# Kernel optimization log

Hardware: AMD Instinct MI355X
Metric: run time of the kernel (lower is better)

## Reference

```python
import jax, jax.numpy as jnp
import numpy as np

N_NODES = 50000
N_EDGES = 800000
EPS = 0.1

def setup_inputs() -> dict:
    key = jax.random.key(0)
    ks = jax.random.split(key, 6)
    x = jax.random.normal(ks[0], (N_NODES, 256), dtype=jnp.float32)
    edge_index = jax.random.randint(ks[1], (2, N_EDGES), 0, N_NODES, dtype=jnp.int64)
    W1 = jax.random.normal(ks[2], (256, 64), dtype=jnp.float32) * (1.0 / np.sqrt(256))
    b1 = jnp.zeros((64,), dtype=jnp.float32)
    att = jax.random.normal(ks[3], (2, 1, 64), dtype=jnp.float32) * (1.0 / np.sqrt(64))
    W2 = jax.random.normal(ks[4], (64, 16), dtype=jnp.float32) * (1.0 / np.sqrt(64))
    b2 = jnp.zeros((16,), dtype=jnp.float32)
    return {"x": x, "edge_index": edge_index, "W1": W1, "b1": b1, "att": att, "W2": W2, "b2": b2}

def _fagcn_conv(x, row, col, norm, att_l, eps):
    # message: norm * x_j gathered at source (row), scatter-add to target (col)
    msg = norm[:, None] * x[row]                      # [E_tot, H]
    x_l = jax.ops.segment_sum(msg, col, num_segments=N_NODES)  # low-pass
    x_h = -eps * x_l                                   # high-pass message = -eps * low message
    gate = jax.nn.sigmoid(jnp.sum(x * att_l, axis=-1, keepdims=True))  # [N,1]
    return gate * x_l + (1.0 - gate) * x_h

def reference(x, edge_index, W1, b1, att, W2, b2):
    # add self loops once (same edge set is reused by every layer)
    loops = jnp.arange(N_NODES, dtype=edge_index.dtype)
    row = jnp.concatenate([edge_index[0], loops])
    col = jnp.concatenate([edge_index[1], loops])
    deg = jax.ops.segment_sum(jnp.ones_like(col, dtype=x.dtype), col, num_segments=N_NODES)
    dinv = jnp.where(deg > 0, jax.lax.rsqrt(jnp.maximum(deg, 1e-30)), 0.0)
    norm = dinv[row] * dinv[col]                       # [E_tot]
    # eval mode: dropout is identity
    h = jax.nn.relu(x @ W1 + b1)                       # [N, H]
    for l in range(att.shape[0]):
        h = _fagcn_conv(h, row, col, norm, att[l], EPS)
    return h @ W2 + b2                                 # [N, out]
```

## Files before the change

### kernel.cpp

```cpp
#include <hip/hip_runtime.h>
#include <math.h>

#define N_FEAT_IN 256
#define N_HID 64
#define N_OUT 16
#define EPS 0.1f

typedef short bf16x8 __attribute__((ext_vector_type(8)));
typedef float f32x4 __attribute__((ext_vector_type(4)));

__device__ inline uint pack2(ushort a, ushort b) { return (uint)a | ((uint)b << 16); }

__device__ inline ushort bf16_rne(float x) {
    uint b = __float_as_uint(x);
    b += 0x7fff + ((b >> 16) & 1);
    return (ushort)(b >> 16);
}

__device__ inline float blo(uint u) { return __uint_as_float(u << 16); }
__device__ inline float bhi(uint u) { return __uint_as_float(u & 0xffff0000u); }

__device__ inline void split_bf16(float x, ushort& hi, ushort& lo) {
    uint b = __float_as_uint(x);
    hi = (ushort)(b >> 16);
    float xl = x - __uint_as_float(b & 0xffff0000u);
    lo = (ushort)(__float_as_uint(xl) >> 16);
}


__global__ void zero_int(int* __restrict__ p, int n) {
    int i = blockIdx.x * blockDim.x + threadIdx.x;
    if (i < n) p[i] = 0;
}


__global__ void hist_rank(const int* __restrict__ col, const int* __restrict__ row,
                          int* __restrict__ cnt, uint* __restrict__ rr, int E) {
    int e = blockIdx.x * blockDim.x + threadIdx.x;
    if (e < E) {
        int r = atomicAdd(&cnt[col[e]], 1);
        rr[e] = ((uint)r << 16) | (uint)row[e];
    }
}


__global__ void scan_chunks(const int* __restrict__ cnt, int* __restrict__ rowptr,
                            int* __restrict__ partial, float* __restrict__ dinv, int N) {
    __shared__ int sm[256];
    int tid = threadIdx.x;
    int gid = blockIdx.x * 256 + tid;
    int v = (gid < N) ? cnt[gid] : 0;
    sm[tid] = v;
    __syncthreads();
#pragma unroll
    for (int off = 1; off < 256; off <<= 1) {
        int add = (tid >= off) ? sm[tid - off] : 0;
        __syncthreads();
        sm[tid] += add;
        __syncthreads();
    }
    if (gid < N) {
        rowptr[gid] = sm[tid] - v;
        dinv[gid] = rsqrtf(1.0f + (float)v);
    }
    if (tid == 255) partial[blockIdx.x] = sm[255];
}


__global__ void scan_finish(int* __restrict__ rowptr, const int* __restrict__ partial,
                            int N, int E, int nchunks) {
    __shared__ int sm[256];
    int tid = threadIdx.x;
    sm[tid] = (tid < nchunks) ? partial[tid] : 0;
    __syncthreads();
#pragma unroll
    for (int off = 1; off < 256; off <<= 1) {
        int add = (tid >= off) ? sm[tid - off] : 0;
        __syncthreads();
        sm[tid] += add;
        __syncthreads();
    }
    int boff = (blockIdx.x == 0) ? 0 : sm[blockIdx.x - 1];
    __syncthreads();
    int gid = blockIdx.x * 256 + tid;
    if (gid < N) rowptr[gid] += boff;
    if (gid == 0) rowptr[N] = E;
}


__global__ void csr_scatter_part(const int* __restrict__ col, const uint* __restrict__ rr,
                                 const int* __restrict__ rowptr,
                                 ushort* __restrict__ srcidx, int E, int rangeSz) {
    int r = blockIdx.x & 7;
    int nsl = gridDim.x >> 3;
    int s = blockIdx.x >> 3;
    int lo = r * rangeSz;
    int hi = lo + rangeSz;
    int stride = nsl * blockDim.x;
    for (int e = s * blockDim.x + threadIdx.x; e < E; e += stride) {
        int c = col[e];
        if (c >= lo && c < hi) {
            uint v = rr[e];
            srcidx[rowptr[c] + (v >> 16)] = (ushort)(v & 0xffffu);
        }
    }
}


__global__ __launch_bounds__(256) void gemm1_mfma(const float* __restrict__ x,
                                                  const float* __restrict__ W1,
                                                  const float* __restrict__ b1,
                                                  const float* __restrict__ dinv,
                                                  uint* __restrict__ AsOut,
                                                  int MB, int totalWaves) {
    __shared__ uint4 wh_lds[2048];
    __shared__ uint4 wl_lds[2048];
    int tid = threadIdx.x;
    for (int e = tid; e < 2048; e += 256) {
        int ks = e >> 8;
        int rem = e & 255;
        int nt = rem >> 6;
        int ln = rem & 63;
        int k0 = ks * 32 + ((ln >> 4) << 3);
        int colw = nt * 16 + (ln & 15);
        ushort hi[8], lo[8];
#pragma unroll
        for (int i = 0; i < 8; ++i) {
            float v = W1[(k0 + i) * 64 + colw];
            split_bf16(v, hi[i], lo[i]);
        }
        wh_lds[e] = make_uint4(pack2(hi[0], hi[1]), pack2(hi[2], hi[3]),
                               pack2(hi[4], hi[5]), pack2(hi[6], hi[7]));
        wl_lds[e] = make_uint4(pack2(lo[0], lo[1]), pack2(lo[2], lo[3]),
                               pack2(lo[4], lo[5]), pack2(lo[6], lo[7]));
    }
    __syncthreads();

    int lane = tid & 63;
    int m = lane & 15;
    int kg = lane >> 4;
    int wid = blockIdx.x * 4 + (tid >> 6);
    const bf16x8* whf = reinterpret_cast<const bf16x8*>(wh_lds);
    const bf16x8* wlf = reinterpret_cast<const bf16x8*>(wl_lds);
    float bias[4];
#pragma unroll
    for (int nt = 0; nt < 4; ++nt) bias[nt] = b1[nt * 16 + m];

    auto load_tile = [&](float4* dst, int mbv) {
        const float4* xr = reinterpret_cast<const float4*>(x) +
                           (size_t)(mbv * 16 + m) * 64 + kg * 2;
#pragma unroll
        for (int ks = 0; ks < 8; ++ks) {
            dst[2 * ks]     = xr[ks * 8];
            dst[2 * ks + 1] = xr[ks * 8 + 1];
        }
    };

    int mb = wid;
    if (mb >= MB) return;
    float4 xv[16], xn[16];
    load_tile(xv, mb);

    while (true) {
        int mbn = mb + totalWaves;
        bool has_next = (mbn < MB);
        if (has_next) load_tile(xn, mbn);

        f32x4 acc[4] = {{0.f,0.f,0.f,0.f},{0.f,0.f,0.f,0.f},
                        {0.f,0.f,0.f,0.f},{0.f,0.f,0.f,0.f}};
#pragma unroll
        for (int ks = 0; ks < 8; ++ks) {
            float4 a0 = xv[2 * ks];
            float4 a1 = xv[2 * ks + 1];
            float f[8] = {a0.x, a0.y, a0.z, a0.w, a1.x, a1.y, a1.z, a1.w};
            bf16x8 ah, al;
#pragma unroll
            for (int i = 0; i < 8; ++i) {
                ushort hu, lu;
                split_bf16(f[i], hu, lu);
                ah[i] = (short)hu;
                al[i] = (short)lu;
            }
#pragma unroll
            for (int nt = 0; nt < 4; ++nt) {
                bf16x8 wh = whf[(ks * 4 + nt) * 64 + lane];
                bf16x8 wl = wlf[(ks * 4 + nt) * 64 + lane];
                acc[nt] = __builtin_amdgcn_mfma_f32_16x16x32_bf16(ah, wh, acc[nt], 0, 0, 0);
                acc[nt] = __builtin_amdgcn_mfma_f32_16x16x32_bf16(al, wh, acc[nt], 0, 0, 0);
                acc[nt] = __builtin_amdgcn_mfma_f32_16x16x32_bf16(ah, wl, acc[nt], 0, 0, 0);
            }
        }

        int r0 = mb * 16 + kg * 4;
        float dr[4];
#pragma unroll
        for (int j = 0; j < 4; ++j) dr[j] = dinv[r0 + j];
#pragma unroll
        for (int nt = 0; nt < 4; ++nt) {
#pragma unroll
            for (int j = 0; j < 4; ++j) {
                float v = fmaxf(acc[nt][j] + bias[nt], 0.0f) * dr[j];
                float p = __shfl_xor(v, 1, 64);
                if ((m & 1) == 0) {
                    uint u = pack2(bf16_rne(v), bf16_rne(p));
                    AsOut[(size_t)(r0 + j) * 32 + ((nt * 16 + m) >> 1)] = u;
                }
            }
        }

        if (!has_next) break;
#pragma unroll
        for (int u = 0; u < 16; ++u) xv[u] = xn[u];
        mb = mbn;
    }
}


template <bool LAST>
__global__ __launch_bounds__(256) void fagcn_layer(
    const uint4* __restrict__ As4, uint4* __restrict__ Out4,
    const float* __restrict__ dinv, const int* __restrict__ rowptr,
    const ushort* __restrict__ src, const float* __restrict__ att_l,
    const float* __restrict__ W2, const float* __restrict__ b2,
    float* __restrict__ out, int N) {
    __shared__ float W2s[64 * 16];
    __shared__ float hL[32 * 68];
    int tid = threadIdx.x;
    if (LAST) {
        for (int e = tid; e < 64 * 16; e += 256) W2s[e] = W2[e];
        __syncthreads();
    }
    int sub = tid & 7;
    int lnode = tid >> 3;
    int i = blockIdx.x * 32 + lnode;
    if (i >= N) i = N - 1;

    int start = rowptr[i];
    int end = rowptr[i + 1];
    const uint4* Ab = As4 + sub;
    uint4 su = Ab[(size_t)i * 8];
    float s0 = blo(su.x), s1 = bhi(su.x), s2 = blo(su.y), s3 = bhi(su.y);
    float s4 = blo(su.z), s5 = bhi(su.z), s6 = blo(su.w), s7 = bhi(su.w);

    float aA0=0.f,aA1=0.f,aA2=0.f,aA3=0.f,aA4=0.f,aA5=0.f,aA6=0.f,aA7=0.f;
    float aB0=0.f,aB1=0.f,aB2=0.f,aB3=0.f,aB4=0.f,aB5=0.f,aB6=0.f,aB7=0.f;
    int j = start;
    for (; j + 7 < end; j += 8) {
        int e0 = src[j];
        int e1 = src[j + 1];
        int e2 = src[j + 2];
        int e3 = src[j + 3];
        int e4 = src[j + 4];
        int e5 = src[j + 5];
        int e6 = src[j + 6];
        int e7 = src[j + 7];
        uint4 u0 = Ab[(size_t)e0 * 8];
        uint4 u1 = Ab[(size_t)e1 * 8];
        uint4 u2 = Ab[(size_t)e2 * 8];
        uint4 u3 = Ab[(size_t)e3 * 8];
        uint4 u4 = Ab[(size_t)e4 * 8];
        uint4 u5 = Ab[(size_t)e5 * 8];
        uint4 u6 = Ab[(size_t)e6 * 8];
        uint4 u7 = Ab[(size_t)e7 * 8];
        aA0 += blo(u0.x); aA1 += bhi(u0.x); aA2 += blo(u0.y); aA3 += bhi(u0.y);
        aA4 += blo(u0.z); aA5 += bhi(u0.z); aA6 += blo(u0.w); aA7 += bhi(u0.w);
        aB0 += blo(u1.x); aB1 += bhi(u1.x); aB2 += blo(u1.y); aB3 += bhi(u1.y);
        aB4 += blo(u1.z); aB5 += bhi(u1.z); aB6 += blo(u1.w); aB7 += bhi(u1.w);
        aA0 += blo(u2.x); aA1 += bhi(u2.x); aA2 += blo(u2.y); aA3 += bhi(u2.y);
        aA4 += blo(u2.z); aA5 += bhi(u2.z); aA6 += blo(u2.w); aA7 += bhi(u2.w);
        aB0 += blo(u3.x); aB1 += bhi(u3.x); aB2 += blo(u3.y); aB3 += bhi(u3.y);
        aB4 += blo(u3.z); aB5 += bhi(u3.z); aB6 += blo(u3.w); aB7 += bhi(u3.w);
        aA0 += blo(u4.x); aA1 += bhi(u4.x); aA2 += blo(u4.y); aA3 += bhi(u4.y);
        aA4 += blo(u4.z); aA5 += bhi(u4.z); aA6 += blo(u4.w); aA7 += bhi(u4.w);
        aB0 += blo(u5.x); aB1 += bhi(u5.x); aB2 += blo(u5.y); aB3 += bhi(u5.y);
        aB4 += blo(u5.z); aB5 += bhi(u5.z); aB6 += blo(u5.w); aB7 += bhi(u5.w);
        aA0 += blo(u6.x); aA1 += bhi(u6.x); aA2 += blo(u6.y); aA3 += bhi(u6.y);
        aA4 += blo(u6.z); aA5 += bhi(u6.z); aA6 += blo(u6.w); aA7 += bhi(u6.w);
        aB0 += blo(u7.x); aB1 += bhi(u7.x); aB2 += blo(u7.y); aB3 += bhi(u7.y);
        aB4 += blo(u7.z); aB5 += bhi(u7.z); aB6 += blo(u7.w); aB7 += bhi(u7.w);
    }
    for (; j + 3 < end; j += 4) {
        int e0 = src[j];
        int e1 = src[j + 1];
        int e2 = src[j + 2];
        int e3 = src[j + 3];
        uint4 u0 = Ab[(size_t)e0 * 8];
        uint4 u1 = Ab[(size_t)e1 * 8];
        uint4 u2 = Ab[(size_t)e2 * 8];
        uint4 u3 = Ab[(size_t)e3 * 8];
        aA0 += blo(u0.x); aA1 += bhi(u0.x); aA2 += blo(u0.y); aA3 += bhi(u0.y);
        aA4 += blo(u0.z); aA5 += bhi(u0.z); aA6 += blo(u0.w); aA7 += bhi(u0.w);
        aB0 += blo(u1.x); aB1 += bhi(u1.x); aB2 += blo(u1.y); aB3 += bhi(u1.y);
        aB4 += blo(u1.z); aB5 += bhi(u1.z); aB6 += blo(u1.w); aB7 += bhi(u1.w);
        aA0 += blo(u2.x); aA1 += bhi(u2.x); aA2 += blo(u2.y); aA3 += bhi(u2.y);
        aA4 += blo(u2.z); aA5 += bhi(u2.z); aA6 += blo(u2.w); aA7 += bhi(u2.w);
        aB0 += blo(u3.x); aB1 += bhi(u3.x); aB2 += blo(u3.y); aB3 += bhi(u3.y);
        aB4 += blo(u3.z); aB5 += bhi(u3.z); aB6 += blo(u3.w); aB7 += bhi(u3.w);
    }
    for (; j < end; ++j) {
        int s = src[j];
        uint4 u = Ab[(size_t)s * 8];
        aA0 += blo(u.x); aA1 += bhi(u.x); aA2 += blo(u.y); aA3 += bhi(u.y);
        aA4 += blo(u.z); aA5 += bhi(u.z); aA6 += blo(u.w); aA7 += bhi(u.w);
    }
    float c0 = aA0 + aB0, c1 = aA1 + aB1, c2 = aA2 + aB2, c3 = aA3 + aB3;
    float c4 = aA4 + aB4, c5 = aA5 + aB5, c6 = aA6 + aB6, c7 = aA7 + aB7;

    float d = dinv[i];
    float4 at0 = reinterpret_cast<const float4*>(att_l)[2 * sub];
    float4 at1 = reinterpret_cast<const float4*>(att_l)[2 * sub + 1];
    float prod = s0 * at0.x + s1 * at0.y + s2 * at0.z + s3 * at0.w +
                 s4 * at1.x + s5 * at1.y + s6 * at1.z + s7 * at1.w;
#pragma unroll
    for (int off = 4; off > 0; off >>= 1)
        prod += __shfl_xor(prod, off, 64);
    float gate = 1.0f / (1.0f + expf(-prod / d));
    float factor = gate * (1.0f + EPS) - EPS;
    float df = d * factor;
    float h0 = df * (c0 + s0), h1 = df * (c1 + s1);
    float h2 = df * (c2 + s2), h3 = df * (c3 + s3);
    float h4 = df * (c4 + s4), h5 = df * (c5 + s5);
    float h6 = df * (c6 + s6), h7 = df * (c7 + s7);

    if (!LAST) {
        Out4[(size_t)i * 8 + sub] =
            make_uint4(pack2(bf16_rne(d * h0), bf16_rne(d * h1)),
                       pack2(bf16_rne(d * h2), bf16_rne(d * h3)),
                       pack2(bf16_rne(d * h4), bf16_rne(d * h5)),
                       pack2(bf16_rne(d * h6), bf16_rne(d * h7)));
    } else {
        float4* hrow4 = reinterpret_cast<float4*>(&hL[lnode * 68]);
        hrow4[2 * sub]     = make_float4(h0, h1, h2, h3);
        hrow4[2 * sub + 1] = make_float4(h4, h5, h6, h7);
        __syncthreads();
        const float4* h4p = reinterpret_cast<const float4*>(&hL[lnode * 68]);
        float accA = b2[sub];
        float accB = b2[sub + 8];
#pragma unroll
        for (int k4 = 0; k4 < 16; ++k4) {
            float4 hv = h4p[k4];
            int k = 4 * k4;
            accA = fmaf(hv.x, W2s[(k + 0) * 16 + sub], accA);
            accB = fmaf(hv.x, W2s[(k + 0) * 16 + sub + 8], accB);
            accA = fmaf(hv.y, W2s[(k + 1) * 16 + sub], accA);
            accB = fmaf(hv.y, W2s[(k + 1) * 16 + sub + 8], accB);
            accA = fmaf(hv.z, W2s[(k + 2) * 16 + sub], accA);
            accB = fmaf(hv.z, W2s[(k + 2) * 16 + sub + 8], accB);
            accA = fmaf(hv.w, W2s[(k + 3) * 16 + sub], accA);
            accB = fmaf(hv.w, W2s[(k + 3) * 16 + sub + 8], accB);
        }
        out[(size_t)i * 16 + sub] = accA;
        out[(size_t)i * 16 + sub + 8] = accB;
    }
}

extern "C" void kernel_launch(void* const* d_in, const int* in_sizes, int n_in,
                              void* d_out, int out_size, void* d_ws, size_t ws_size,
                              hipStream_t stream) {
    const float* x   = (const float*)d_in[0];
    const int*   ei  = (const int*)d_in[1];
    const float* W1  = (const float*)d_in[2];
    const float* b1  = (const float*)d_in[3];
    const float* att = (const float*)d_in[4];
    const float* W2  = (const float*)d_in[5];
    const float* b2  = (const float*)d_in[6];
    float* out = (float*)d_out;

    const int N = in_sizes[0] / N_FEAT_IN;
    const int E = in_sizes[1] / 2;
    const int L = in_sizes[4] / N_HID;

    const int* row = ei;
    const int* col = ei + E;

    char* wp = (char*)d_ws;
    auto alloc = [&](size_t bytes) -> char* {
        char* p = wp;
        wp += (bytes + 255) & ~(size_t)255;
        return p;
    };
    float*  dinv    = (float*)alloc((size_t)N * 4);
    int*    cnt     = (int*)alloc((size_t)N * 4);
    int*    rowptr  = (int*)alloc((size_t)(N + 1) * 4);
    uint*   rr      = (uint*)alloc((size_t)E * 4);
    int*    partial = (int*)alloc(256 * 4);
    ushort* srcidx  = (ushort*)alloc((size_t)E * 2);
    uint*   AsA     = (uint*)alloc((size_t)N * 32 * 4);
    uint*   AsB     = (uint*)alloc((size_t)N * 32 * 4);

    const int TB = 256;
    const int nchunks = (N + TB - 1) / TB;
    const int rangeSz = (N + 7) / 8;
    const int PART_GRID = 1024;

    zero_int<<<(N + TB - 1) / TB, TB, 0, stream>>>(cnt, N);
    hist_rank<<<(E + TB - 1) / TB, TB, 0, stream>>>(col, row, cnt, rr, E);
    scan_chunks<<<nchunks, TB, 0, stream>>>(cnt, rowptr, partial, dinv, N);
    scan_finish<<<nchunks, TB, 0, stream>>>(rowptr, partial, N, E, nchunks);
    csr_scatter_part<<<PART_GRID, TB, 0, stream>>>(col, rr, rowptr, srcidx, E, rangeSz);

    {
        const int blocks = 512;
        const int MB = N / 16;
        gemm1_mfma<<<blocks, TB, 0, stream>>>(x, W1, b1, dinv, AsA, MB, blocks * 4);
    }

    {
        int grid = (N + 31) / 32;
        uint4* A = (uint4*)AsA;
        uint4* B = (uint4*)AsB;
        for (int l = 0; l < L; ++l) {
            const float* att_l = att + (size_t)l * N_HID;
            if (l == L - 1) {
                fagcn_layer<true><<<grid, TB, 0, stream>>>(
                    A, B, dinv, rowptr, srcidx, att_l, W2, b2, out, N);
            } else {
                fagcn_layer<false><<<grid, TB, 0, stream>>>(
                    A, B, dinv, rowptr, srcidx, att_l, W2, b2, out, N);
                uint4* tmp = A; A = B; B = tmp;
            }
        }
    }
}
```

Baseline: 132.8 us.

## Sort nodes by in-degree so each wave aggregates similar-degree neighbourhoods

```diff
diff --git a/kernel.cpp b/kernel.cpp
--- a/kernel.cpp
+++ b/kernel.cpp
@@ -5,6 +5,7 @@
 #define N_HID 64
 #define N_OUT 16
 #define EPS 0.1f
+#define NBINS 1024
 
 typedef short bf16x8 __attribute__((ext_vector_type(8)));
 typedef float f32x4 __attribute__((ext_vector_type(4)));
@@ -45,11 +46,16 @@
 
 
 __global__ void scan_chunks(const int* __restrict__ cnt, int* __restrict__ rowptr,
-                            int* __restrict__ partial, float* __restrict__ dinv, int N) {
+                            int* __restrict__ partial, float* __restrict__ dinv,
+                            int* __restrict__ dhist, int N) {
     __shared__ int sm[256];
+    __shared__ int h[NBINS];
     int tid = threadIdx.x;
+    for (int b = tid; b < NBINS; b += 256) h[b] = 0;
+    __syncthreads();
     int gid = blockIdx.x * 256 + tid;
     int v = (gid < N) ? cnt[gid] : 0;
+    if (gid < N) atomicAdd(&h[min(v, NBINS - 1)], 1);
     sm[tid] = v;
     __syncthreads();
 #pragma unroll
@@ -64,6 +70,9 @@
         dinv[gid] = rsqrtf(1.0f + (float)v);
     }
     if (tid == 255) partial[blockIdx.x] = sm[255];
+    __syncthreads();
+    for (int b = tid; b < NBINS; b += 256)
+        if (h[b]) atomicAdd(&dhist[b], h[b]);
 }
 
 
@@ -85,6 +94,53 @@
     int gid = blockIdx.x * 256 + tid;
     if (gid < N) rowptr[gid] += boff;
     if (gid == 0) rowptr[N] = E;
+}
+
+
+__global__ void deg_scan(int* __restrict__ dhist) {
+    __shared__ int sums[256];
+    int t = threadIdx.x;
+    int v0 = dhist[4 * t], v1 = dhist[4 * t + 1];
+    int v2 = dhist[4 * t + 2], v3 = dhist[4 * t + 3];
+    int s = v0 + v1 + v2 + v3;
+    sums[t] = s;
+    __syncthreads();
+#pragma unroll
+    for (int off = 1; off < 256; off <<= 1) {
+        int add = (t >= off) ? sums[t - off] : 0;
+        __syncthreads();
+        sums[t] += add;
+        __syncthreads();
+    }
+    int excl = sums[t] - s;
+    dhist[4 * t]     = excl;
+    dhist[4 * t + 1] = excl + v0;
+    dhist[4 * t + 2] = excl + v0 + v1;
+    dhist[4 * t + 3] = excl + v0 + v1 + v2;
+}
+
+
+__global__ void perm_scatter(const int* __restrict__ cnt, int* __restrict__ dbase,
+                             int* __restrict__ perm, int N) {
+    __shared__ int h[NBINS];
+    __shared__ int hb[NBINS];
+    int tid = threadIdx.x;
+    for (int b = tid; b < NBINS; b += 256) h[b] = 0;
+    __syncthreads();
+    int gid = blockIdx.x * 256 + tid;
+    int d = 0, myrank = 0;
+    bool valid = (gid < N);
+    if (valid) {
+        d = min(cnt[gid], NBINS - 1);
+        myrank = atomicAdd(&h[d], 1);
+    }
+    __syncthreads();
+    for (int b = tid; b < NBINS; b += 256) {
+        int c = h[b];
+        hb[b] = c ? atomicAdd(&dbase[b], c) : 0;
+    }
+    __syncthreads();
+    if (valid) perm[hb[d] + myrank] = gid;
 }
 
 
@@ -220,7 +276,8 @@
 __global__ __launch_bounds__(256) void fagcn_layer(
     const uint4* __restrict__ As4, uint4* __restrict__ Out4,
     const float* __restrict__ dinv, const int* __restrict__ rowptr,
-    const ushort* __restrict__ src, const float* __restrict__ att_l,
+    const ushort* __restrict__ src, const int* __restrict__ perm,
+    const float* __restrict__ att_l,
     const float* __restrict__ W2, const float* __restrict__ b2,
     float* __restrict__ out, int N) {
     __shared__ float W2s[64 * 16];
@@ -232,8 +289,9 @@
     }
     int sub = tid & 7;
     int lnode = tid >> 3;
-    int i = blockIdx.x * 32 + lnode;
-    if (i >= N) i = N - 1;
+    int gid = blockIdx.x * 32 + lnode;
+    if (gid >= N) gid = N - 1;
+    int i = perm[gid];
 
     int start = rowptr[i];
     int end = rowptr[i + 1];
@@ -245,40 +303,6 @@
     float aA0=0.f,aA1=0.f,aA2=0.f,aA3=0.f,aA4=0.f,aA5=0.f,aA6=0.f,aA7=0.f;
     float aB0=0.f,aB1=0.f,aB2=0.f,aB3=0.f,aB4=0.f,aB5=0.f,aB6=0.f,aB7=0.f;
     int j = start;
-    for (; j + 7 < end; j += 8) {
-        int e0 = src[j];
-        int e1 = src[j + 1];
-        int e2 = src[j + 2];
-        int e3 = src[j + 3];
-        int e4 = src[j + 4];
-        int e5 = src[j + 5];
-        int e6 = src[j + 6];
-        int e7 = src[j + 7];
-        uint4 u0 = Ab[(size_t)e0 * 8];
-        uint4 u1 = Ab[(size_t)e1 * 8];
-        uint4 u2 = Ab[(size_t)e2 * 8];
-        uint4 u3 = Ab[(size_t)e3 * 8];
-        uint4 u4 = Ab[(size_t)e4 * 8];
-        uint4 u5 = Ab[(size_t)e5 * 8];
-        uint4 u6 = Ab[(size_t)e6 * 8];
-        uint4 u7 = Ab[(size_t)e7 * 8];
-        aA0 += blo(u0.x); aA1 += bhi(u0.x); aA2 += blo(u0.y); aA3 += bhi(u0.y);
-        aA4 += blo(u0.z); aA5 += bhi(u0.z); aA6 += blo(u0.w); aA7 += bhi(u0.w);
-        aB0 += blo(u1.x); aB1 += bhi(u1.x); aB2 += blo(u1.y); aB3 += bhi(u1.y);
-        aB4 += blo(u1.z); aB5 += bhi(u1.z); aB6 += blo(u1.w); aB7 += bhi(u1.w);
-        aA0 += blo(u2.x); aA1 += bhi(u2.x); aA2 += blo(u2.y); aA3 += bhi(u2.y);
-        aA4 += blo(u2.z); aA5 += bhi(u2.z); aA6 += blo(u2.w); aA7 += bhi(u2.w);
-        aB0 += blo(u3.x); aB1 += bhi(u3.x); aB2 += blo(u3.y); aB3 += bhi(u3.y);
-        aB4 += blo(u3.z); aB5 += bhi(u3.z); aB6 += blo(u3.w); aB7 += bhi(u3.w);
-        aA0 += blo(u4.x); aA1 += bhi(u4.x); aA2 += blo(u4.y); aA3 += bhi(u4.y);
-        aA4 += blo(u4.z); aA5 += bhi(u4.z); aA6 += blo(u4.w); aA7 += bhi(u4.w);
-        aB0 += blo(u5.x); aB1 += bhi(u5.x); aB2 += blo(u5.y); aB3 += bhi(u5.y);
-        aB4 += blo(u5.z); aB5 += bhi(u5.z); aB6 += blo(u5.w); aB7 += bhi(u5.w);
-        aA0 += blo(u6.x); aA1 += bhi(u6.x); aA2 += blo(u6.y); aA3 += bhi(u6.y);
-        aA4 += blo(u6.z); aA5 += bhi(u6.z); aA6 += blo(u6.w); aA7 += bhi(u6.w);
-        aB0 += blo(u7.x); aB1 += bhi(u7.x); aB2 += blo(u7.y); aB3 += bhi(u7.y);
-        aB4 += blo(u7.z); aB5 += bhi(u7.z); aB6 += blo(u7.w); aB7 += bhi(u7.w);
-    }
     for (; j + 3 < end; j += 4) {
         int e0 = src[j];
         int e1 = src[j + 1];
@@ -380,10 +404,12 @@
         return p;
     };
     float*  dinv    = (float*)alloc((size_t)N * 4);
-    int*    cnt     = (int*)alloc((size_t)N * 4);
+    int*    cnt     = (int*)alloc((size_t)(N + NBINS) * 4);
+    int*    dhist   = cnt + N;
     int*    rowptr  = (int*)alloc((size_t)(N + 1) * 4);
     uint*   rr      = (uint*)alloc((size_t)E * 4);
     int*    partial = (int*)alloc(256 * 4);
+    int*    perm    = (int*)alloc((size_t)N * 4);
     ushort* srcidx  = (ushort*)alloc((size_t)E * 2);
     uint*   AsA     = (uint*)alloc((size_t)N * 32 * 4);
     uint*   AsB     = (uint*)alloc((size_t)N * 32 * 4);
@@ -393,10 +419,12 @@
     const int rangeSz = (N + 7) / 8;
     const int PART_GRID = 1024;
 
-    zero_int<<<(N + TB - 1) / TB, TB, 0, stream>>>(cnt, N);
+    zero_int<<<(N + NBINS + TB - 1) / TB, TB, 0, stream>>>(cnt, N + NBINS);
     hist_rank<<<(E + TB - 1) / TB, TB, 0, stream>>>(col, row, cnt, rr, E);
-    scan_chunks<<<nchunks, TB, 0, stream>>>(cnt, rowptr, partial, dinv, N);
+    scan_chunks<<<nchunks, TB, 0, stream>>>(cnt, rowptr, partial, dinv, dhist, N);
     scan_finish<<<nchunks, TB, 0, stream>>>(rowptr, partial, N, E, nchunks);
+    deg_scan<<<1, TB, 0, stream>>>(dhist);
+    perm_scatter<<<nchunks, TB, 0, stream>>>(cnt, dhist, perm, N);
     csr_scatter_part<<<PART_GRID, TB, 0, stream>>>(col, rr, rowptr, srcidx, E, rangeSz);
 
     {
@@ -413,10 +441,10 @@
             const float* att_l = att + (size_t)l * N_HID;
             if (l == L - 1) {
                 fagcn_layer<true><<<grid, TB, 0, stream>>>(
-                    A, B, dinv, rowptr, srcidx, att_l, W2, b2, out, N);
+                    A, B, dinv, rowptr, srcidx, perm, att_l, W2, b2, out, N);
             } else {
                 fagcn_layer<false><<<grid, TB, 0, stream>>>(
-                    A, B, dinv, rowptr, srcidx, att_l, W2, b2, out, N);
+                    A, B, dinv, rowptr, srcidx, perm, att_l, W2, b2, out, N);
                 uint4* tmp = A; A = B; B = tmp;
             }
         }
```

Result: slower. 136.2 us (median of 2 runs) (+2.6%).
